# Kernel tuning notes

Hardware: AMD Instinct MI355X
Metric: run time of the kernel (lower is better)

The kernel has to match this reference:

```python
import jax, jax.numpy as jnp
import numpy as np

B, N, M, C = 8, 2048, 2048, 256
EPS = 1e-8  # torch.cosine_similarity norm clamp


def setup_inputs() -> dict:
    key = jax.random.key(0)
    k1, k2, k3 = jax.random.split(key, 3)
    x1 = jax.random.normal(k1, (B, N, C), dtype=jnp.float32)
    x2 = jax.random.normal(k2, (B, M, C), dtype=jnp.float32)
    # labels in {-1, 0, 1}; force diagonal to 1 so every batch has both +1 and -1
    z = jax.random.randint(k3, (B, N, M), 0, 3).astype(jnp.int64) - 1
    idx = jnp.arange(min(N, M))
    z = z.at[:, idx, idx].set(1)
    t = jnp.asarray(10.0, dtype=jnp.float32)
    b = jnp.asarray(-10.0, dtype=jnp.float32)
    return {"z": z, "x1": x1, "x2": x2, "t": t, "b": b}


def reference(z, x1, x2, t, b):
    # batch filter: keep batches containing both a positive and a negative pair
    B_mask = jnp.any(z == -1, axis=(1, 2)) & jnp.any(z == 1, axis=(1, 2))
    # cosine similarity via normalize + GEMM (instead of [B,N,M,C] broadcast)
    n1 = x1 / jnp.maximum(jnp.linalg.norm(x1, axis=-1, keepdims=True), EPS)
    n2 = x2 / jnp.maximum(jnp.linalg.norm(x2, axis=-1, keepdims=True), EPS)
    cos_sim = jnp.einsum("bnc,bmc->bnm", n1, n2)  # [B, N, M]
    zf = z.astype(jnp.float32)
    y = zf * (t * cos_sim - b)
    valid = (B_mask[:, None, None] & (z != 0)).astype(jnp.float32)
    # masked mean == mean over filtered batches & nonzero labels
    loss = -(jax.nn.log_sigmoid(y) * valid).sum() / valid.sum()
    return loss
```

## Files before the change

### kernel.cpp

```cpp
#include <hip/hip_runtime.h>
#include <hip/hip_bf16.h>
#include <stdint.h>

#define BB 8
#define NN 2048
#define MM 2048
#define CC 256

typedef __attribute__((ext_vector_type(8))) short short8;
typedef __attribute__((ext_vector_type(4))) float f32x4;

__device__ __forceinline__ void gl_lds16(const void* g, void* l) {
    __builtin_amdgcn_global_load_lds(
        (const __attribute__((address_space(1))) void*)g,
        (__attribute__((address_space(3))) void*)l, 16, 0, 0);
}

__device__ __forceinline__ unsigned short f2bf(float f) {
    __hip_bfloat16 h = __float2bfloat16(f);
    return *reinterpret_cast<unsigned short*>(&h);
}

__global__ __launch_bounds__(256) void norm_cast_kernel(
    const float* __restrict__ x1, const float* __restrict__ x2,
    char* __restrict__ outA, char* __restrict__ outB,
    float* __restrict__ lsum, unsigned int* __restrict__ vcnt,
    unsigned int* __restrict__ flags, unsigned int* __restrict__ done) {
    if (blockIdx.x == 0 && threadIdx.x < 8) {
        int t = threadIdx.x;
        lsum[t] = 0.0f; vcnt[t] = 0u; flags[t] = 0u; flags[BB + t] = 0u;
        if (t == 0) *done = 0u;
    }
    int gwave = (blockIdx.x * blockDim.x + threadIdx.x) >> 6;
    int lane  = threadIdx.x & 63;
    bool isA = gwave < BB * NN;
    const float* src = isA ? x1 : x2;
    int row = isA ? gwave : gwave - BB * NN;
    float4 v = reinterpret_cast<const float4*>(src + (size_t)row * CC)[lane];
    float ss = v.x * v.x + v.y * v.y + v.z * v.z + v.w * v.w;
#pragma unroll
    for (int off = 32; off; off >>= 1) ss += __shfl_xor(ss, off);
    float inv = 1.0f / fmaxf(sqrtf(ss), 1e-8f);
    ushort4 h;
    h.x = f2bf(v.x * inv); h.y = f2bf(v.y * inv);
    h.z = f2bf(v.z * inv); h.w = f2bf(v.w * inv);
    int c   = lane >> 3;
    int kb  = (lane >> 1) & 3;
    int kbL = kb ^ ((row >> 1) & 3);
    char* p;
    if (isA) {
        p = outA + (size_t)row * 512 + c * 64 + kbL * 16 + (lane & 1) * 8;
    } else {
        int b = row >> 11, r = row & 2047;
        p = outB + (size_t)b * 1048576 + (size_t)((r >> 4) * 8 + c) * 1024
                 + kbL * 256 + (r & 15) * 16 + (lane & 1) * 8;
    }
    *reinterpret_cast<ushort4*>(p) = h;
}

__global__ __launch_bounds__(512) void fused_mfma_kernel(
    const int*  __restrict__ z,
    const char* __restrict__ nA, const char* __restrict__ nB,
    const float* __restrict__ tptr, const float* __restrict__ bptr,
    float* __restrict__ lsum, unsigned int* __restrict__ vcnt,
    unsigned int* __restrict__ flags, unsigned int* __restrict__ done,
    float* __restrict__ out) {

    __shared__ __align__(16) char ldsA[65536];
    __shared__ float        s_sum[8];
    __shared__ unsigned int s_cnt[8];
    __shared__ unsigned int s_flag[2];

    const int flat = blockIdx.x;
    const int b    = flat & 7;
    const int rest = flat >> 3;
    const int n0   = (rest & 15) * 128;
    const int mq   = rest >> 4;
    const int tid  = threadIdx.x, lane = tid & 63, wid = tid >> 6;
    const int wr = wid >> 2, wc = wid & 3, l15 = lane & 15;
    const int q4  = (lane >> 4) << 2;
    const int kbL = (lane >> 4) ^ ((l15 >> 1) & 3);

    {
        const char* src = nA + ((size_t)b * NN + n0) * 512
                        + (size_t)(lane >> 2) * 512 + wid * 64 + (lane & 3) * 16;
        char* dst = ldsA + wid * 8192;
#pragma unroll
        for (int g = 0; g < 8; g++)
            gl_lds16(src + (size_t)g * 8192, dst + g * 1024);
    }

    const char* gB0 = nB + (size_t)b * 1048576 + (size_t)mq * 262144
                    + kbL * 256 + l15 * 16;
    const int* zb = z + ((size_t)b * NN + n0 + wr * 64 + q4) * MM
                      + mq * 512 + wc * 32 + l15;

    const float tv = *tptr;
    const float bs = *bptr;
    const float LOG2E = 1.4426950408889634f;
    const float LN2   = 0.6931471805599453f;

    __syncthreads();

    float lsu = 0.0f;
    int   lcnt = 0;
    int   mxz = -1, mnz = 1;

#pragma unroll
    for (int mt = 0; mt < 4; mt++) {
        const char* gBt = gB0 + mt * 65536;

        short8 bfr[8][2];
#pragma unroll
        for (int c = 0; c < 8; c++)
#pragma unroll
            for (int n = 0; n < 2; n++)
                bfr[c][n] = *reinterpret_cast<const short8*>(
                    gBt + (wc * 2 + n) * 8192 + c * 1024);

        int zr[32];
#pragma unroll
        for (int m = 0; m < 4; m++)
#pragma unroll
            for (int r = 0; r < 4; r++)
#pragma unroll
                for (int n = 0; n < 2; n++)
                    zr[(m * 4 + r) * 2 + n] = zb[mt * 128 + (m * 16 + r) * MM + n * 16];

        __builtin_amdgcn_sched_barrier(0);

        f32x4 acc[4][2] = {};
#pragma unroll
        for (int c = 0; c < 8; c++) {
            short8 af[4];
#pragma unroll
            for (int m = 0; m < 4; m++)
                af[m] = *reinterpret_cast<const short8*>(
                    ldsA + c * 8192 + (wr * 64 + m * 16 + l15) * 64 + kbL * 16);
#pragma unroll
            for (int m = 0; m < 4; m++) {
                acc[m][0] = __builtin_amdgcn_mfma_f32_16x16x32_bf16(af[m], bfr[c][0], acc[m][0], 0, 0, 0);
                acc[m][1] = __builtin_amdgcn_mfma_f32_16x16x32_bf16(af[m], bfr[c][1], acc[m][1], 0, 0, 0);
            }
        }

#pragma unroll
        for (int m = 0; m < 4; m++)
#pragma unroll
            for (int r = 0; r < 4; r++)
#pragma unroll
                for (int n = 0; n < 2; n++) {
                    int zij = zr[(m * 4 + r) * 2 + n];
                    float cs = acc[m][n][r];
                    float pp = fmaf(tv, cs, -bs);
                    float y  = (zij < 0) ? -pp : pp;
                    float e  = __builtin_amdgcn_exp2f(-fabsf(y) * LOG2E);
                    float lg = __builtin_amdgcn_logf(1.0f + e);
                    float ls = fminf(y, 0.0f) - LN2 * lg;
                    if (zij != 0) { lsu += ls; lcnt++; }
                    mxz = max(mxz, zij); mnz = min(mnz, zij);
                }
    }

#pragma unroll
    for (int off = 32; off; off >>= 1) {
        lsu  += __shfl_down(lsu, off);
        lcnt += __shfl_down(lcnt, off);
    }
    unsigned long long mp = __ballot(mxz > 0);
    unsigned long long mn = __ballot(mnz < 0);

    __syncthreads();
    if (tid < 2) s_flag[tid] = 0u;
    __syncthreads();
    if (lane == 0) {
        s_sum[wid] = lsu;
        s_cnt[wid] = (unsigned int)lcnt;
        if (mp) atomicOr(&s_flag[0], 1u);
        if (mn) atomicOr(&s_flag[1], 1u);
    }
    __syncthreads();
    if (tid == 0) {
        float ts = 0.f; unsigned int tc = 0u;
#pragma unroll
        for (int w = 0; w < 8; w++) { ts += s_sum[w]; tc += s_cnt[w]; }
        atomicAdd(&lsum[b], ts);
        atomicAdd(&vcnt[b], tc);
        if (s_flag[0]) atomicOr(&flags[b], 1u);
        if (s_flag[1]) atomicOr(&flags[BB + b], 1u);
        __threadfence();
        unsigned int old = atomicAdd(done, 1u);
        if (old == gridDim.x - 1) {
            __threadfence();
            double s = 0.0, c = 0.0;
#pragma unroll
            for (int bb = 0; bb < BB; bb++) {
                unsigned int fp = atomicOr(&flags[bb], 0u);
                unsigned int fn = atomicOr(&flags[BB + bb], 0u);
                float        sv = atomicAdd(&lsum[bb], 0.0f);
                unsigned int cv = atomicAdd(&vcnt[bb], 0u);
                if (fp && fn) { s += (double)sv; c += (double)cv; }
            }
            out[0] = (float)(-s / c);
        }
    }
}

extern "C" void kernel_launch(void* const* d_in, const int* in_sizes, int n_in,
                              void* d_out, int out_size, void* d_ws, size_t ws_size,
                              hipStream_t stream) {
    const int*   z   = (const int*)  d_in[0];
    const float* x1  = (const float*)d_in[1];
    const float* x2  = (const float*)d_in[2];
    const float* tp  = (const float*)d_in[3];
    const float* bp  = (const float*)d_in[4];
    float* out = (float*)d_out;

    char* ws = (char*)d_ws;
    char*  normA = ws;
    char*  normB = ws + (size_t)BB * NN * 512;
    char*  accb  = ws + (size_t)BB * (NN + MM) * 512;
    float*        lsum  = (float*)accb;
    unsigned int* vcnt  = (unsigned int*)(accb + 64);
    unsigned int* flags = (unsigned int*)(accb + 128);
    unsigned int* done  = (unsigned int*)(accb + 256);

    hipLaunchKernelGGL(norm_cast_kernel, dim3(BB * (NN + MM) / 4), dim3(256), 0, stream,
                       x1, x2, normA, normB, lsum, vcnt, flags, done);

    hipLaunchKernelGGL(fused_mfma_kernel, dim3(512), dim3(512), 0, stream,
                       z, normA, normB, tp, bp, lsum, vcnt, flags, done, out);
}
```

Before: 63.45 us.

## Pre-pack labels into 2-bit codes in the normalize kernel, consume them in GEMM

```diff
diff --git a/kernel.cpp b/kernel.cpp
--- a/kernel.cpp
+++ b/kernel.cpp
@@ -21,45 +21,90 @@
     return *reinterpret_cast<unsigned short*>(&h);
 }
 
-__global__ __launch_bounds__(256) void norm_cast_kernel(
+__global__ __launch_bounds__(512) void stream_kernel(
+    const int* __restrict__ z,
     const float* __restrict__ x1, const float* __restrict__ x2,
     char* __restrict__ outA, char* __restrict__ outB,
+    uint2* __restrict__ codes,
     float* __restrict__ lsum, unsigned int* __restrict__ vcnt,
     unsigned int* __restrict__ flags, unsigned int* __restrict__ done) {
-    if (blockIdx.x == 0 && threadIdx.x < 8) {
-        int t = threadIdx.x;
-        lsum[t] = 0.0f; vcnt[t] = 0u; flags[t] = 0u; flags[BB + t] = 0u;
-        if (t == 0) *done = 0u;
-    }
-    int gwave = (blockIdx.x * blockDim.x + threadIdx.x) >> 6;
-    int lane  = threadIdx.x & 63;
-    bool isA = gwave < BB * NN;
-    const float* src = isA ? x1 : x2;
-    int row = isA ? gwave : gwave - BB * NN;
-    float4 v = reinterpret_cast<const float4*>(src + (size_t)row * CC)[lane];
-    float ss = v.x * v.x + v.y * v.y + v.z * v.z + v.w * v.w;
-#pragma unroll
-    for (int off = 32; off; off >>= 1) ss += __shfl_xor(ss, off);
-    float inv = 1.0f / fmaxf(sqrtf(ss), 1e-8f);
-    ushort4 h;
-    h.x = f2bf(v.x * inv); h.y = f2bf(v.y * inv);
-    h.z = f2bf(v.z * inv); h.w = f2bf(v.w * inv);
-    int c   = lane >> 3;
-    int kb  = (lane >> 1) & 3;
-    int kbL = kb ^ ((row >> 1) & 3);
-    char* p;
-    if (isA) {
-        p = outA + (size_t)row * 512 + c * 64 + kbL * 16 + (lane & 1) * 8;
+
+    __shared__ int zt[128 * 132];
+    const int bid = blockIdx.x;
+    const int tid = threadIdx.x;
+
+    if (bid == 0 && tid < 8) {
+        lsum[tid] = 0.0f; vcnt[tid] = 0u; flags[tid] = 0u; flags[BB + tid] = 0u;
+        if (tid == 0) *done = 0u;
+    }
+
+    if (bid < 2048) {
+        const int b  = bid & 7;
+        const int r2 = bid >> 3;
+        const int by = r2 & 15;
+        const int bx = r2 >> 4;
+        const int n0 = by * 128, m0 = bx * 128;
+
+#pragma unroll
+        for (int i = 0; i < 8; i++) {
+            int idx = i * 512 + tid;
+            int row = idx >> 5;
+            int col = (idx & 31) * 4;
+            int4 v = *reinterpret_cast<const int4*>(
+                z + ((size_t)b * NN + n0 + row) * MM + m0 + col);
+            *reinterpret_cast<int4*>(&zt[row * 132 + col]) = v;
+        }
+        __syncthreads();
+
+        const int lane = tid & 63, wid = tid >> 6;
+        const int wr = wid >> 2, wc = wid & 3;
+        const int l15 = lane & 15, q4 = (lane >> 4) << 2;
+
+        uint32_t w0 = 0u, w1 = 0u;
+#pragma unroll
+        for (int m = 0; m < 4; m++)
+#pragma unroll
+            for (int r = 0; r < 4; r++)
+#pragma unroll
+                for (int n = 0; n < 2; n++) {
+                    int v = zt[(wr * 64 + m * 16 + q4 + r) * 132 + wc * 32 + l15 + n * 16];
+                    uint32_t code = (v == 0) ? 0u : ((v > 0) ? 1u : 2u);
+                    int s = (m * 4 + r) * 2 + n;
+                    if (s < 16) w0 |= code << (s * 2);
+                    else        w1 |= code << ((s - 16) * 2);
+                }
+        codes[(size_t)((b * 16 + by) * 16 + bx) * 512 + tid] = make_uint2(w0, w1);
     } else {
-        int b = row >> 11, r = row & 2047;
-        p = outB + (size_t)b * 1048576 + (size_t)((r >> 4) * 8 + c) * 1024
-                 + kbL * 256 + (r & 15) * 16 + (lane & 1) * 8;
-    }
-    *reinterpret_cast<ushort4*>(p) = h;
+        int gwave = ((bid - 2048) << 3) + (tid >> 6);
+        int lane  = tid & 63;
+        bool isA = gwave < BB * NN;
+        const float* src = isA ? x1 : x2;
+        int row = isA ? gwave : gwave - BB * NN;
+        float4 v = reinterpret_cast<const float4*>(src + (size_t)row * CC)[lane];
+        float ss = v.x * v.x + v.y * v.y + v.z * v.z + v.w * v.w;
+#pragma unroll
+        for (int off = 32; off; off >>= 1) ss += __shfl_xor(ss, off);
+        float inv = 1.0f / fmaxf(sqrtf(ss), 1e-8f);
+        ushort4 h;
+        h.x = f2bf(v.x * inv); h.y = f2bf(v.y * inv);
+        h.z = f2bf(v.z * inv); h.w = f2bf(v.w * inv);
+        int c   = lane >> 3;
+        int kb  = (lane >> 1) & 3;
+        int kbL = kb ^ ((row >> 1) & 3);
+        char* p;
+        if (isA) {
+            p = outA + (size_t)row * 512 + c * 64 + kbL * 16 + (lane & 1) * 8;
+        } else {
+            int b = row >> 11, r = row & 2047;
+            p = outB + (size_t)b * 1048576 + (size_t)((r >> 4) * 8 + c) * 1024
+                     + kbL * 256 + (r & 15) * 16 + (lane & 1) * 8;
+        }
+        *reinterpret_cast<ushort4*>(p) = h;
+    }
 }
 
 __global__ __launch_bounds__(512) void fused_mfma_kernel(
-    const int*  __restrict__ z,
+    const uint2* __restrict__ codes,
     const char* __restrict__ nA, const char* __restrict__ nB,
     const float* __restrict__ tptr, const float* __restrict__ bptr,
     float* __restrict__ lsum, unsigned int* __restrict__ vcnt,
@@ -74,11 +119,11 @@
     const int flat = blockIdx.x;
     const int b    = flat & 7;
     const int rest = flat >> 3;
-    const int n0   = (rest & 15) * 128;
+    const int ny   = rest & 15;
+    const int n0   = ny * 128;
     const int mq   = rest >> 4;
     const int tid  = threadIdx.x, lane = tid & 63, wid = tid >> 6;
     const int wr = wid >> 2, wc = wid & 3, l15 = lane & 15;
-    const int q4  = (lane >> 4) << 2;
     const int kbL = (lane >> 4) ^ ((l15 >> 1) & 3);
 
     {
@@ -92,8 +137,6 @@
 
     const char* gB0 = nB + (size_t)b * 1048576 + (size_t)mq * 262144
                     + kbL * 256 + l15 * 16;
-    const int* zb = z + ((size_t)b * NN + n0 + wr * 64 + q4) * MM
-                      + mq * 512 + wc * 32 + l15;
 
     const float tv = *tptr;
     const float bs = *bptr;
@@ -104,11 +147,13 @@
 
     float lsu = 0.0f;
     int   lcnt = 0;
-    int   mxz = -1, mnz = 1;
+    bool  anyp = false, anyn = false;
 
 #pragma unroll
     for (int mt = 0; mt < 4; mt++) {
         const char* gBt = gB0 + mt * 65536;
+
+        uint2 zc = codes[(size_t)((b * 16 + ny) * 16 + (mq * 4 + mt)) * 512 + tid];
 
         short8 bfr[8][2];
 #pragma unroll
@@ -117,15 +162,6 @@
             for (int n = 0; n < 2; n++)
                 bfr[c][n] = *reinterpret_cast<const short8*>(
                     gBt + (wc * 2 + n) * 8192 + c * 1024);
-
-        int zr[32];
-#pragma unroll
-        for (int m = 0; m < 4; m++)
-#pragma unroll
-            for (int r = 0; r < 4; r++)
-#pragma unroll
-                for (int n = 0; n < 2; n++)
-                    zr[(m * 4 + r) * 2 + n] = zb[mt * 128 + (m * 16 + r) * MM + n * 16];
 
         __builtin_amdgcn_sched_barrier(0);
 
@@ -150,15 +186,18 @@
             for (int r = 0; r < 4; r++)
 #pragma unroll
                 for (int n = 0; n < 2; n++) {
-                    int zij = zr[(m * 4 + r) * 2 + n];
+                    int s = (m * 4 + r) * 2 + n;
+                    uint32_t word = (s < 16) ? zc.x : zc.y;
+                    uint32_t code = (word >> ((s & 15) * 2)) & 3u;
                     float cs = acc[m][n][r];
                     float pp = fmaf(tv, cs, -bs);
-                    float y  = (zij < 0) ? -pp : pp;
+                    float y  = (code == 2u) ? -pp : pp;
                     float e  = __builtin_amdgcn_exp2f(-fabsf(y) * LOG2E);
                     float lg = __builtin_amdgcn_logf(1.0f + e);
                     float ls = fminf(y, 0.0f) - LN2 * lg;
-                    if (zij != 0) { lsu += ls; lcnt++; }
-                    mxz = max(mxz, zij); mnz = min(mnz, zij);
+                    if (code) { lsu += ls; lcnt++; }
+                    anyp |= (code == 1u);
+                    anyn |= (code == 2u);
                 }
     }
 
@@ -167,8 +206,8 @@
         lsu  += __shfl_down(lsu, off);
         lcnt += __shfl_down(lcnt, off);
     }
-    unsigned long long mp = __ballot(mxz > 0);
-    unsigned long long mn = __ballot(mnz < 0);
+    unsigned long long mp = __ballot(anyp);
+    unsigned long long mn = __ballot(anyn);
 
     __syncthreads();
     if (tid < 2) s_flag[tid] = 0u;
@@ -219,15 +258,16 @@
     char* ws = (char*)d_ws;
     char*  normA = ws;
     char*  normB = ws + (size_t)BB * NN * 512;
-    char*  accb  = ws + (size_t)BB * (NN + MM) * 512;
+    uint2* codes = (uint2*)(ws + (size_t)BB * (NN + MM) * 512);
+    char*  accb  = ws + (size_t)BB * (NN + MM) * 512 + (size_t)8 * 1024 * 1024;
     float*        lsum  = (float*)accb;
     unsigned int* vcnt  = (unsigned int*)(accb + 64);
     unsigned int* flags = (unsigned int*)(accb + 128);
     unsigned int* done  = (unsigned int*)(accb + 256);
 
-    hipLaunchKernelGGL(norm_cast_kernel, dim3(BB * (NN + MM) / 4), dim3(256), 0, stream,
-                       x1, x2, normA, normB, lsum, vcnt, flags, done);
+    hipLaunchKernelGGL(stream_kernel, dim3(6144), dim3(512), 0, stream,
+                       z, x1, x2, normA, normB, codes, lsum, vcnt, flags, done);
 
     hipLaunchKernelGGL(fused_mfma_kernel, dim3(512), dim3(512), 0, stream,
-                       z, normA, normB, tp, bp, lsum, vcnt, flags, done, out);
-}
+                       codes, normA, normB, tp, bp, lsum, vcnt, flags, done, out);
+}
```

New measurement: 82.97 us. 1.31x slower.
